# Kernel optimization log

Hardware: AMD Instinct MI355X
Metric: run time of the kernel (lower is better)

Reference implementation:

```python
import jax, jax.numpy as jnp
import numpy as np

S, B, D, V = 1024, 8, 512, 8000


def _ln(x, g, b, eps=1e-5):
    m = x.mean(-1, keepdims=True)
    v = x.var(-1, keepdims=True)
    return (x - m) / jnp.sqrt(v + eps) * g + b


def setup_inputs() -> dict:
    key = jax.random.key(0)
    ks = jax.random.split(key, 8)
    representation = jax.random.normal(ks[0], (S, B, D), jnp.float32)
    # CTC-style logits: tokens come in runs of ~4 frames so argmax has segments
    tok = jax.random.randint(ks[1], (S // 4, B), 0, V)
    tok = jnp.repeat(tok, 4, axis=0)  # [S,B]
    logit = jax.random.normal(ks[2], (S, B, V), jnp.float32) + 6.0 * jax.nn.one_hot(tok, V, dtype=jnp.float32)
    padding = jnp.zeros((B, S), bool)  # all frames valid
    # linear_adapter: Linear(D,2D) -> ReLU -> Linear(2D,D) -> LayerNorm
    w1 = jax.random.normal(ks[3], (2 * D, D), jnp.float32) * (D ** -0.5)
    b1 = jnp.zeros((2 * D,), jnp.float32)
    w2 = jax.random.normal(ks[4], (D, 2 * D), jnp.float32) * ((2 * D) ** -0.5)
    b2 = jnp.zeros((D,), jnp.float32)
    ln1_g = jnp.ones((D,), jnp.float32)
    ln1_b = jnp.zeros((D,), jnp.float32)
    # embed_adapter weight [dict_size, dim], init std = dim**-0.5
    emb_w = jax.random.normal(ks[5], (V, D), jnp.float32) * (D ** -0.5)
    eln_g = jnp.ones((D,), jnp.float32)
    eln_b = jnp.zeros((D,), jnp.float32)
    return dict(representation=representation, logit=logit, padding=padding,
                w1=w1, b1=b1, w2=w2, b2=b2, ln1_g=ln1_g, ln1_b=ln1_b,
                emb_w=emb_w, eln_g=eln_g, eln_b=eln_b)


def reference(representation, logit, padding, w1, b1, w2, b2, ln1_g, ln1_b, emb_w, eln_g, eln_b):
    # distribution = softmax(logit / T), T = 1.0
    dist = jax.nn.softmax(logit, axis=-1)  # [S,B,V]
    # linear adapter: Linear -> ReLU -> Linear -> LN
    h = jax.nn.relu(jnp.einsum('sbd,ed->sbe', representation, w1) + b1)
    linear_out = _ln(jnp.einsum('sbe,de->sbd', h, w2) + b2, ln1_g, ln1_b)
    # context adapter: dist @ embed_adapter.weight, then embed LN
    soft_out = _ln(jnp.einsum('sbv,vd->sbd', dist, emb_w), eln_g, eln_b)
    out = linear_out + soft_out  # league
    # --- CTC 'avg' compress (shrink), vectorized; output padded to S frames ---
    pred = jnp.argmax(dist, axis=-1).T  # [B,S]
    valid = ~padding  # [B,S]
    prev = jnp.concatenate([jnp.full((pred.shape[0], 1), -1, pred.dtype), pred[:, :-1]], axis=1)
    change = (pred != prev) & valid  # segment starts
    seg = jnp.cumsum(change, axis=1) - 1  # segment id per frame
    seg = jnp.where(valid, seg, S)  # invalid frames -> out-of-range id
    # weights_matrix[b, t, s] = 1/len(segment s) if frame t in segment s
    onehot = (seg[:, :, None] == jnp.arange(S)[None, None, :]).astype(out.dtype)  # [B,S,S]
    counts = onehot.sum(1)  # [B,S] frames per segment
    w = onehot * jnp.where(counts > 0, 1.0 / counts, 0.0)[:, None, :]
    # representation.permute(1,2,0).bmm(weights).permute(2,0,1)
    compressed = jnp.einsum('sbd,bst->tbd', out, w)  # [S_new(padded to S), B, D]
    new_lengths = change.sum(1)
    new_padding = jnp.arange(S)[None, :] >= new_lengths[:, None]
    return compressed, new_padding
```

## Files before the change

kernel.cpp:

```cpp
#include <hip/hip_runtime.h>
#include <hip/hip_bf16.h>

typedef __attribute__((ext_vector_type(8))) __bf16 bf16x8;
typedef __attribute__((ext_vector_type(4))) __bf16 bf16x4;
typedef __attribute__((ext_vector_type(4))) float  f32x4;

#define AS1 __attribute__((address_space(1)))
#define AS3 __attribute__((address_space(3)))

__global__ __launch_bounds__(256) void k_prep(const float* __restrict__ rep,
                                              const float* __restrict__ w1,
                                              const float* __restrict__ w2,
                                              const float* __restrict__ emb,
                                              __bf16* __restrict__ Xb,
                                              __bf16* __restrict__ w1b,
                                              __bf16* __restrict__ w2b,
                                              __bf16* __restrict__ embP) {
  int bid = blockIdx.x;
  if (bid < 5120) {
    const float* in; __bf16* out; int i;
    if (bid < 4096)      { in = rep; out = Xb;  i = bid * 256 + threadIdx.x; }
    else if (bid < 4608) { in = w1;  out = w1b; i = (bid - 4096) * 256 + threadIdx.x; }
    else                 { in = w2;  out = w2b; i = (bid - 4608) * 256 + threadIdx.x; }
    float4 f = reinterpret_cast<const float4*>(in)[i];
    bf16x4 o = { (__bf16)f.x, (__bf16)f.y, (__bf16)f.z, (__bf16)f.w };
    reinterpret_cast<bf16x4*>(out)[i] = o;
  } else {
    int idx = (bid - 5120) * 256 + threadIdx.x;
    int L = idx & 63;
    int gt = idx >> 6;
    int T = gt % 250, g = gt / 250;
    int kb = T * 32 + (L >> 4) * 8;
    int d  = g * 16 + (L & 15);
    float v[8];
#pragma unroll
    for (int j = 0; j < 8; ++j) v[j] = emb[(size_t)(kb + j) * 512 + d];
    bf16x8 o = {(__bf16)v[0], (__bf16)v[1], (__bf16)v[2], (__bf16)v[3],
                (__bf16)v[4], (__bf16)v[5], (__bf16)v[6], (__bf16)v[7]};
    *(bf16x8*)(embP + (size_t)idx * 8) = o;
  }
}

__global__ __launch_bounds__(512, 4) void k_fused(const float* __restrict__ logit,
                                                  const __bf16* __restrict__ embP,
                                                  __bf16* __restrict__ sofp,
                                                  float* __restrict__ rowsum,
                                                  float* __restrict__ amaxv,
                                                  int* __restrict__ amaxi) {
  __shared__ __align__(16) __bf16 lA[2][64 * 32];
  const int klen = 2016;
  int bid = blockIdx.x;
  int xcd = bid & 7;
  int chunk = xcd >> 1;
  int mb = ((bid >> 3) << 1) | (xcd & 1);
  int k0 = chunk * klen;
  int kn = min(klen, 8000 - k0);
  int nt = kn >> 5;
  int T0 = chunk * 63;
  int tid = threadIdx.x, lane = tid & 63, wid = tid >> 6;
  int ar = tid >> 3, ac = tid & 7;
  const float* lrow = logit + (size_t)(mb * 64 + ar) * 8000 + k0 + ac * 4;
  int awoff = ar * 64 + ((((ac >> 1) ^ ((ar >> 1) & 3)) << 4)) + (ac & 1) * 8;
  f32x4 acc[4][4] = {};
  float sumacc = 0.f, mv = -1e30f; int mi = 0;

  auto exppack = [&](float4 lg, int tt) -> bf16x4 {
    float e[4];
#pragma unroll
    for (int c = 0; c < 4; ++c) {
      float x = (&lg.x)[c];
      if (x > mv) { mv = x; mi = k0 + tt * 32 + ac * 4 + c; }
      e[c] = __expf(x);
      sumacc += e[c];
    }
    return bf16x4{ (__bf16)e[0], (__bf16)e[1], (__bf16)e[2], (__bf16)e[3] };
  };
  bf16x8 bcur[4];
  auto loadB = [&](int TT) {
#pragma unroll
    for (int n = 0; n < 4; ++n)
      bcur[n] = *(const bf16x8*)(embP + ((size_t)((wid * 4 + n) * 250 + TT)) * 512 + lane * 8);
  };

  float4 rb_ = *(const float4*)(lrow);
  float4 rb  = *(const float4*)(lrow + 32);
  loadB(T0);
  bf16x4 e0 = exppack(rb_, 0);
  *(bf16x4*)((char*)(&lA[0][0]) + awoff) = e0;

  int cur = 0;
  for (int t = 0; t < nt; ++t) {
    bool hn = (t + 1 < nt), h2 = (t + 2 < nt);
    float4 rc = rb;
    if (h2) rc = *(const float4*)(lrow + (size_t)(t + 2) * 32);
    asm volatile("s_waitcnt lgkmcnt(0)" ::: "memory");
    __builtin_amdgcn_s_barrier();
    if (hn) {
      bf16x4 e4 = exppack(rb, t + 1);
      *(bf16x4*)((char*)(&lA[cur ^ 1][0]) + awoff) = e4;
    }
    bf16x8 af[4];
#pragma unroll
    for (int m = 0; m < 4; ++m) {
      int r = m * 16 + (lane & 15);
      int s = (lane >> 4) ^ ((r >> 1) & 3);
      af[m] = *(const bf16x8*)((const char*)lA[cur] + r * 64 + s * 16);
    }
    __builtin_amdgcn_s_setprio(1);
#pragma unroll
    for (int m = 0; m < 4; ++m)
#pragma unroll
      for (int n = 0; n < 4; ++n)
        acc[m][n] = __builtin_amdgcn_mfma_f32_16x16x32_bf16(af[m], bcur[n], acc[m][n], 0, 0, 0);
    __builtin_amdgcn_s_setprio(0);
    if (hn) loadB(T0 + t + 1);
    rb = rc;
    cur ^= 1;
  }
#pragma unroll
  for (int o = 1; o <= 4; o <<= 1) {
    sumacc += __shfl_xor(sumacc, o);
    float ov = __shfl_xor(mv, o); int oi = __shfl_xor(mi, o);
    if (ov > mv || (ov == mv && oi < mi)) { mv = ov; mi = oi; }
  }
  int grow = mb * 64 + ar;
  if (ac == 0) {
    rowsum[chunk * 8192 + grow] = sumacc;
    amaxv[chunk * 8192 + grow]  = mv;
    amaxi[chunk * 8192 + grow]  = mi;
  }
  __bf16* Cb = sofp + (size_t)chunk * 8192 * 512;
  int row0 = mb * 64 + ((lane >> 4) << 2);
  int col0 = wid * 64 + (lane & 15);
#pragma unroll
  for (int n = 0; n < 4; ++n) {
    int col = col0 + n * 16;
#pragma unroll
    for (int m = 0; m < 4; ++m)
#pragma unroll
      for (int j = 0; j < 4; ++j)
        Cb[(size_t)(row0 + m * 16 + j) * 512 + col] = (__bf16)acc[m][n][j];
  }
}

template<int EPI>
__global__ __launch_bounds__(256) void k_gemm_bt(const __bf16* __restrict__ A,
                                                 const __bf16* __restrict__ B,
                                                 __bf16* __restrict__ Cb,
                                                 const float* __restrict__ bias,
                                                 int K, int N, int klen, long long ostride) {
  __shared__ __align__(16) __bf16 lA[2][128 * 64];
  __shared__ __align__(16) __bf16 lB[2][128 * 64];
  int tid = threadIdx.x, lane = tid & 63, wid = tid >> 6;
  int wr = wid >> 1, wc = wid & 1;
  int k0 = blockIdx.z * klen;
  int kn = min(klen, K - k0);
  int nt = kn >> 6;
  const __bf16* Ab = A + (size_t)blockIdx.x * 128 * K + k0;
  const __bf16* Bb = B + (size_t)blockIdx.y * 128 * K + k0;
  int sr = tid >> 3, ss = tid & 7;
  f32x4 acc[4][4] = {};

  auto stage = [&](int buf, int kt) {
#pragma unroll
    for (int i = 0; i < 4; ++i) {
      int r = i * 32 + sr;
      int col = kt + ((ss ^ (r & 7)) << 3);
      __builtin_amdgcn_global_load_lds((const AS1 void*)(Ab + (size_t)r * K + col),
                                       (AS3 void*)(&lA[buf][i * 2048 + tid * 8]), 16, 0, 0);
      __builtin_amdgcn_global_load_lds((const AS1 void*)(Bb + (size_t)r * K + col),
                                       (AS3 void*)(&lB[buf][i * 2048 + tid * 8]), 16, 0, 0);
    }
  };

  stage(0, 0);
  __syncthreads();
  int cur = 0;
  for (int t = 0; t < nt; ++t) {
    if (t + 1 < nt) stage(cur ^ 1, (t + 1) << 6);
#pragma unroll
    for (int kk = 0; kk < 2; ++kk) {
      bf16x8 af[4], bv[4];
#pragma unroll
      for (int m = 0; m < 4; ++m) {
        int r = wr * 64 + m * 16 + (lane & 15);
        int slot = ((kk << 2) + (lane >> 4)) ^ (r & 7);
        af[m] = *(const bf16x8*)((const char*)lA[cur] + r * 128 + slot * 16);
      }
#pragma unroll
      for (int n = 0; n < 4; ++n) {
        int r = wc * 64 + n * 16 + (lane & 15);
        int slot = ((kk << 2) + (lane >> 4)) ^ (r & 7);
        bv[n] = *(const bf16x8*)((const char*)lB[cur] + r * 128 + slot * 16);
      }
#pragma unroll
      for (int m = 0; m < 4; ++m)
#pragma unroll
        for (int n = 0; n < 4; ++n)
          acc[m][n] = __builtin_amdgcn_mfma_f32_16x16x32_bf16(af[m], bv[n], acc[m][n], 0, 0, 0);
    }
    __syncthreads();
    cur ^= 1;
  }
  if (EPI == 0) Cb += (size_t)blockIdx.z * (size_t)ostride;
  int row0 = blockIdx.x * 128 + wr * 64 + ((lane >> 4) << 2);
  int col0 = blockIdx.y * 128 + wc * 64 + (lane & 15);
#pragma unroll
  for (int n = 0; n < 4; ++n) {
    int col = col0 + n * 16;
    float bvv = (EPI == 1) ? bias[col] : 0.f;
#pragma unroll
    for (int m = 0; m < 4; ++m) {
#pragma unroll
      for (int j = 0; j < 4; ++j) {
        int row = row0 + m * 16 + j;
        float val = acc[m][n][j] + bvv;
        if (EPI == 1) val = fmaxf(val, 0.f);
        Cb[(size_t)row * N + col] = (__bf16)val;
      }
    }
  }
}

__global__ __launch_bounds__(256) void k_scan(const float* __restrict__ amaxv,
                                              const int* __restrict__ amaxi,
                                              int* __restrict__ seg_start,
                                              int* __restrict__ seg_cnt,
                                              int* __restrict__ new_len,
                                              float* __restrict__ out_pad) {
  __shared__ int lp[8192];
  __shared__ int len_s[8];
  int tid = threadIdx.x;
  for (int i = tid; i < 8192; i += 256) {
    float bv = amaxv[i]; int bi = amaxi[i];
#pragma unroll
    for (int c = 1; c < 4; ++c) {
      float v = amaxv[c * 8192 + i]; int ix = amaxi[c * 8192 + i];
      if (v > bv || (v == bv && ix < bi)) { bv = v; bi = ix; }
    }
    lp[(i & 7) * 1024 + (i >> 3)] = bi;
  }
  __syncthreads();
  if (tid < 8) {
    int b = tid, prev = -1, seg = -1, start = 0;
    const int* row = lp + b * 1024;
    for (int s = 0; s < 1024; ++s) {
      int p = row[s];
      if (p != prev) {
        if (seg >= 0) seg_cnt[b * 1024 + seg] = s - start;
        ++seg; seg_start[b * 1024 + seg] = s; start = s; prev = p;
      }
    }
    seg_cnt[b * 1024 + seg] = 1024 - start;
    len_s[b] = seg + 1;
    new_len[b] = seg + 1;
  }
  __syncthreads();
  for (int i = tid; i < 8192; i += 256) {
    int b = i >> 10, s = i & 1023;
    out_pad[b * 1024 + s] = (s >= len_s[b]) ? 1.f : 0.f;
  }
}

__global__ __launch_bounds__(256) void k_compress(const __bf16* __restrict__ lin,
                                                  const __bf16* __restrict__ sof,
                                                  const float* __restrict__ rowsum,
                                                  const float* __restrict__ bias2,
                                                  const float* __restrict__ g1, const float* __restrict__ b1,
                                                  const float* __restrict__ g2, const float* __restrict__ b2,
                                                  const int* __restrict__ seg_start,
                                                  const int* __restrict__ seg_cnt,
                                                  const int* __restrict__ new_len,
                                                  float* __restrict__ comp) {
  const long long P = (long long)8192 * 512;
  int wid = threadIdx.x >> 6, lane = threadIdx.x & 63;
  int t = blockIdx.x * 4 + wid, b = blockIdx.y;
  float* dst = comp + ((size_t)(t * 8 + b)) * 512 + lane * 8;
  int len = new_len[b];
  if (t >= len) {
    f32x4 z = {0.f, 0.f, 0.f, 0.f};
    *(f32x4*)dst = z; *(f32x4*)(dst + 4) = z;
    return;
  }
  int s0i = seg_start[b * 1024 + t], cnt = seg_cnt[b * 1024 + t];
  int d8 = lane * 8;
  float gg1[8], bbv1[8], gg2[8], bbv2[8], bb2v[8];
#pragma unroll
  for (int k = 0; k < 8; ++k) {
    gg1[k] = g1[d8 + k]; bbv1[k] = b1[d8 + k];
    gg2[k] = g2[d8 + k]; bbv2[k] = b2[d8 + k];
    bb2v[k] = bias2[d8 + k];
  }
  f32x4 a0 = {0.f, 0.f, 0.f, 0.f}, a1 = {0.f, 0.f, 0.f, 0.f};
  for (int s = s0i; s < s0i + cnt; ++s) {
    int row = s * 8 + b;
    size_t base = (size_t)row * 512 + d8;
    float invd = 1.f / (rowsum[row] + rowsum[8192 + row] + rowsum[16384 + row] + rowsum[24576 + row]);
    bf16x8 l0 = *(const bf16x8*)(lin + base);
    bf16x8 l1 = *(const bf16x8*)(lin + P + base);
    bf16x8 t0 = *(const bf16x8*)(sof + base);
    bf16x8 t1 = *(const bf16x8*)(sof + P + base);
    bf16x8 t2 = *(const bf16x8*)(sof + 2 * P + base);
    bf16x8 t3 = *(const bf16x8*)(sof + 3 * P + base);
    float x[8], y[8];
#pragma unroll
    for (int k = 0; k < 8; ++k) {
      x[k] = (float)l0[k] + (float)l1[k] + bb2v[k];
      y[k] = ((float)t0[k] + (float)t1[k] + (float)t2[k] + (float)t3[k]) * invd;
    }
    float sx = 0, qx = 0, sy = 0, qy = 0;
#pragma unroll
    for (int k = 0; k < 8; ++k) { sx += x[k]; qx += x[k] * x[k]; sy += y[k]; qy += y[k] * y[k]; }
#pragma unroll
    for (int o = 32; o; o >>= 1) {
      sx += __shfl_xor(sx, o); qx += __shfl_xor(qx, o);
      sy += __shfl_xor(sy, o); qy += __shfl_xor(qy, o);
    }
    const float invD = 1.f / 512.f;
    float mx = sx * invD, vx = qx * invD - mx * mx;
    float my = sy * invD, vy = qy * invD - my * my;
    float rx = rsqrtf(vx + 1e-5f), ry = rsqrtf(vy + 1e-5f);
#pragma unroll
    for (int k = 0; k < 8; ++k) {
      float o8 = (x[k] - mx) * rx * gg1[k] + bbv1[k] + (y[k] - my) * ry * gg2[k] + bbv2[k];
      if (k < 4) a0[k] += o8; else a1[k - 4] += o8;
    }
  }
  float inv = 1.f / (float)cnt;
  a0 *= inv; a1 *= inv;
  *(f32x4*)dst = a0; *(f32x4*)(dst + 4) = a1;
}

extern "C" void kernel_launch(void* const* d_in, const int* in_sizes, int n_in,
                              void* d_out, int out_size, void* d_ws, size_t ws_size,
                              hipStream_t stream) {
  const float* rep   = (const float*)d_in[0];
  const float* logit = (const float*)d_in[1];
  const float* w1    = (const float*)d_in[3];
  const float* b1    = (const float*)d_in[4];
  const float* w2    = (const float*)d_in[5];
  const float* b2    = (const float*)d_in[6];
  const float* g1    = (const float*)d_in[7];
  const float* bb1   = (const float*)d_in[8];
  const float* emb   = (const float*)d_in[9];
  const float* g2    = (const float*)d_in[10];
  const float* bb2   = (const float*)d_in[11];
  float* out = (float*)d_out;
  (void)in_sizes; (void)n_in; (void)out_size; (void)ws_size;

  char* ws = (char*)d_ws;
  size_t off = 0;
  auto alloc = [&](size_t bytes) -> void* {
    void* p = ws + off; off += (bytes + 255) & ~(size_t)255; return p;
  };
  const long long P = (long long)8192 * 512;
  __bf16* Xb    = (__bf16*)alloc((size_t)P * 2);
  __bf16* w1b   = (__bf16*)alloc((size_t)1024 * 512 * 2);
  __bf16* w2b   = (__bf16*)alloc((size_t)512 * 1024 * 2);
  __bf16* embP  = (__bf16*)alloc((size_t)512 * 8000 * 2);
  __bf16* Hb    = (__bf16*)alloc((size_t)8192 * 1024 * 2);
  __bf16* linp  = (__bf16*)alloc((size_t)P * 2 * 2);
  __bf16* sofp  = (__bf16*)alloc((size_t)P * 2 * 4);
  float*  rowsm = (float*)alloc((size_t)4 * 8192 * 4);
  float*  amv   = (float*)alloc((size_t)4 * 8192 * 4);
  int*    ami   = (int*)alloc((size_t)4 * 8192 * 4);
  int*    segs  = (int*)alloc((size_t)8192 * 4);
  int*    segc  = (int*)alloc((size_t)8192 * 4);
  int*    nlen  = (int*)alloc(64);

  k_prep<<<7120, 256, 0, stream>>>(rep, w1, w2, emb, Xb, w1b, w2b, embP);
  k_fused<<<512, 512, 0, stream>>>(logit, embP, sofp, rowsm, amv, ami);
  k_gemm_bt<1><<<dim3(64, 8, 1), 256, 0, stream>>>(Xb, w1b, Hb, b1, 512, 1024, 512, 0);
  k_gemm_bt<0><<<dim3(64, 4, 2), 256, 0, stream>>>(Hb, w2b, linp, nullptr, 1024, 512, 512, P);
  k_scan<<<1, 256, 0, stream>>>(amv, ami, segs, segc, nlen, out + (size_t)8192 * 512);
  k_compress<<<dim3(256, 8), 256, 0, stream>>>(linp, sofp, rowsm, b2, g1, bb1, g2, bb2,
                                               segs, segc, nlen, out);
}
```

Before: 281.7 us.

## Horizontally fuse softmax-embed GEMM with GEMM1, and GEMM2 with segment scan

Merges the independent kernels into shared launches. The fused softmax/embedding GEMM and the first adapter GEMM become one kernel, with blocks alternating between the two roles. The second GEMM and the argmax segment scan become another kernel, where block 0 runs the scan. This cuts launch count and per-kernel tail gaps, and lets compute-bound GEMM work overlap with the bandwidth-bound logit stream. In exchange every block of the first kernel now reserves 64KB of LDS, even the softmax path that needed only 8KB. That may reduce resident blocks per CU for the dominant logit-streaming work. GEMM1 is also retiled for 512 threads.

Measured after the change: 326.4 us. 1.16x slower.

```diff
diff --git a/kernel.cpp b/kernel.cpp
--- a/kernel.cpp
+++ b/kernel.cpp
@@ -41,224 +41,299 @@
   }
 }
 
-__global__ __launch_bounds__(512, 4) void k_fused(const float* __restrict__ logit,
-                                                  const __bf16* __restrict__ embP,
-                                                  __bf16* __restrict__ sofp,
-                                                  float* __restrict__ rowsum,
-                                                  float* __restrict__ amaxv,
-                                                  int* __restrict__ amaxi) {
-  __shared__ __align__(16) __bf16 lA[2][64 * 32];
-  const int klen = 2016;
+__global__ __launch_bounds__(512, 4) void k_fgA(const float* __restrict__ logit,
+                                                const __bf16* __restrict__ embP,
+                                                __bf16* __restrict__ sofp,
+                                                float* __restrict__ rowsum,
+                                                float* __restrict__ amaxv,
+                                                int* __restrict__ amaxi,
+                                                const __bf16* __restrict__ Xb,
+                                                const __bf16* __restrict__ w1b,
+                                                __bf16* __restrict__ Hb,
+                                                const float* __restrict__ b1) {
+  __shared__ __align__(16) __bf16 smem[4][128 * 64];
   int bid = blockIdx.x;
-  int xcd = bid & 7;
-  int chunk = xcd >> 1;
-  int mb = ((bid >> 3) << 1) | (xcd & 1);
-  int k0 = chunk * klen;
-  int kn = min(klen, 8000 - k0);
-  int nt = kn >> 5;
-  int T0 = chunk * 63;
   int tid = threadIdx.x, lane = tid & 63, wid = tid >> 6;
-  int ar = tid >> 3, ac = tid & 7;
-  const float* lrow = logit + (size_t)(mb * 64 + ar) * 8000 + k0 + ac * 4;
-  int awoff = ar * 64 + ((((ac >> 1) ^ ((ar >> 1) & 3)) << 4)) + (ac & 1) * 8;
-  f32x4 acc[4][4] = {};
-  float sumacc = 0.f, mv = -1e30f; int mi = 0;
-
-  auto exppack = [&](float4 lg, int tt) -> bf16x4 {
-    float e[4];
-#pragma unroll
-    for (int c = 0; c < 4; ++c) {
-      float x = (&lg.x)[c];
-      if (x > mv) { mv = x; mi = k0 + tt * 32 + ac * 4 + c; }
-      e[c] = __expf(x);
-      sumacc += e[c];
-    }
-    return bf16x4{ (__bf16)e[0], (__bf16)e[1], (__bf16)e[2], (__bf16)e[3] };
-  };
-  bf16x8 bcur[4];
-  auto loadB = [&](int TT) {
-#pragma unroll
-    for (int n = 0; n < 4; ++n)
-      bcur[n] = *(const bf16x8*)(embP + ((size_t)((wid * 4 + n) * 250 + TT)) * 512 + lane * 8);
-  };
-
-  float4 rb_ = *(const float4*)(lrow);
-  float4 rb  = *(const float4*)(lrow + 32);
-  loadB(T0);
-  bf16x4 e0 = exppack(rb_, 0);
-  *(bf16x4*)((char*)(&lA[0][0]) + awoff) = e0;
-
-  int cur = 0;
-  for (int t = 0; t < nt; ++t) {
-    bool hn = (t + 1 < nt), h2 = (t + 2 < nt);
-    float4 rc = rb;
-    if (h2) rc = *(const float4*)(lrow + (size_t)(t + 2) * 32);
-    asm volatile("s_waitcnt lgkmcnt(0)" ::: "memory");
-    __builtin_amdgcn_s_barrier();
-    if (hn) {
-      bf16x4 e4 = exppack(rb, t + 1);
-      *(bf16x4*)((char*)(&lA[cur ^ 1][0]) + awoff) = e4;
-    }
-    bf16x8 af[4];
-#pragma unroll
-    for (int m = 0; m < 4; ++m) {
-      int r = m * 16 + (lane & 15);
-      int s = (lane >> 4) ^ ((r >> 1) & 3);
-      af[m] = *(const bf16x8*)((const char*)lA[cur] + r * 64 + s * 16);
-    }
-    __builtin_amdgcn_s_setprio(1);
-#pragma unroll
-    for (int m = 0; m < 4; ++m)
+  int grp = bid >> 3;
+  int sub = ((grp >> 1) << 3) | (bid & 7);
+
+  if ((grp & 1) == 0) {
+    char* lAb = (char*)&smem[0][0];
+    const int klen = 2016;
+    int xcd = sub & 7;
+    int chunk = xcd >> 1;
+    int mb = ((sub >> 3) << 1) | (xcd & 1);
+    int k0 = chunk * klen;
+    int kn = min(klen, 8000 - k0);
+    int nt = kn >> 5;
+    int T0 = chunk * 63;
+    int ar = tid >> 3, ac = tid & 7;
+    const float* lrow = logit + (size_t)(mb * 64 + ar) * 8000 + k0 + ac * 4;
+    int awoff = ar * 64 + ((((ac >> 1) ^ ((ar >> 1) & 3)) << 4)) + (ac & 1) * 8;
+    f32x4 acc[4][4] = {};
+    float sumacc = 0.f, mv = -1e30f; int mi = 0;
+
+    auto exppack = [&](float4 lg, int tt) -> bf16x4 {
+      float e[4];
+#pragma unroll
+      for (int c = 0; c < 4; ++c) {
+        float x = (&lg.x)[c];
+        if (x > mv) { mv = x; mi = k0 + tt * 32 + ac * 4 + c; }
+        e[c] = __expf(x);
+        sumacc += e[c];
+      }
+      return bf16x4{ (__bf16)e[0], (__bf16)e[1], (__bf16)e[2], (__bf16)e[3] };
+    };
+    bf16x8 bcur[4];
+    auto loadB = [&](int TT) {
 #pragma unroll
       for (int n = 0; n < 4; ++n)
-        acc[m][n] = __builtin_amdgcn_mfma_f32_16x16x32_bf16(af[m], bcur[n], acc[m][n], 0, 0, 0);
-    __builtin_amdgcn_s_setprio(0);
-    if (hn) loadB(T0 + t + 1);
-    rb = rc;
-    cur ^= 1;
-  }
-#pragma unroll
-  for (int o = 1; o <= 4; o <<= 1) {
-    sumacc += __shfl_xor(sumacc, o);
-    float ov = __shfl_xor(mv, o); int oi = __shfl_xor(mi, o);
-    if (ov > mv || (ov == mv && oi < mi)) { mv = ov; mi = oi; }
-  }
-  int grow = mb * 64 + ar;
-  if (ac == 0) {
-    rowsum[chunk * 8192 + grow] = sumacc;
-    amaxv[chunk * 8192 + grow]  = mv;
-    amaxi[chunk * 8192 + grow]  = mi;
-  }
-  __bf16* Cb = sofp + (size_t)chunk * 8192 * 512;
-  int row0 = mb * 64 + ((lane >> 4) << 2);
-  int col0 = wid * 64 + (lane & 15);
-#pragma unroll
-  for (int n = 0; n < 4; ++n) {
-    int col = col0 + n * 16;
-#pragma unroll
-    for (int m = 0; m < 4; ++m)
-#pragma unroll
-      for (int j = 0; j < 4; ++j)
-        Cb[(size_t)(row0 + m * 16 + j) * 512 + col] = (__bf16)acc[m][n][j];
+        bcur[n] = *(const bf16x8*)(embP + ((size_t)((wid * 4 + n) * 250 + TT)) * 512 + lane * 8);
+    };
+
+    float4 rb_ = *(const float4*)(lrow);
+    float4 rb  = *(const float4*)(lrow + 32);
+    loadB(T0);
+    bf16x4 e0 = exppack(rb_, 0);
+    *(bf16x4*)(lAb + awoff) = e0;
+
+    int cur = 0;
+    for (int t = 0; t < nt; ++t) {
+      bool hn = (t + 1 < nt), h2 = (t + 2 < nt);
+      float4 rc = rb;
+      if (h2) rc = *(const float4*)(lrow + (size_t)(t + 2) * 32);
+      asm volatile("s_waitcnt lgkmcnt(0)" ::: "memory");
+      __builtin_amdgcn_s_barrier();
+      if (hn) {
+        bf16x4 e4 = exppack(rb, t + 1);
+        *(bf16x4*)(lAb + (cur ^ 1) * 4096 + awoff) = e4;
+      }
+      bf16x8 af[4];
+#pragma unroll
+      for (int m = 0; m < 4; ++m) {
+        int r = m * 16 + (lane & 15);
+        int s = (lane >> 4) ^ ((r >> 1) & 3);
+        af[m] = *(const bf16x8*)(lAb + cur * 4096 + r * 64 + s * 16);
+      }
+      __builtin_amdgcn_s_setprio(1);
+#pragma unroll
+      for (int m = 0; m < 4; ++m)
+#pragma unroll
+        for (int n = 0; n < 4; ++n)
+          acc[m][n] = __builtin_amdgcn_mfma_f32_16x16x32_bf16(af[m], bcur[n], acc[m][n], 0, 0, 0);
+      __builtin_amdgcn_s_setprio(0);
+      if (hn) loadB(T0 + t + 1);
+      rb = rc;
+      cur ^= 1;
+    }
+#pragma unroll
+    for (int o = 1; o <= 4; o <<= 1) {
+      sumacc += __shfl_xor(sumacc, o);
+      float ov = __shfl_xor(mv, o); int oi = __shfl_xor(mi, o);
+      if (ov > mv || (ov == mv && oi < mi)) { mv = ov; mi = oi; }
+    }
+    int grow = mb * 64 + ar;
+    if (ac == 0) {
+      rowsum[chunk * 8192 + grow] = sumacc;
+      amaxv[chunk * 8192 + grow]  = mv;
+      amaxi[chunk * 8192 + grow]  = mi;
+    }
+    __bf16* Cb = sofp + (size_t)chunk * 8192 * 512;
+    int row0 = mb * 64 + ((lane >> 4) << 2);
+    int col0 = wid * 64 + (lane & 15);
+#pragma unroll
+    for (int n = 0; n < 4; ++n) {
+      int col = col0 + n * 16;
+#pragma unroll
+      for (int m = 0; m < 4; ++m)
+#pragma unroll
+        for (int j = 0; j < 4; ++j)
+          Cb[(size_t)(row0 + m * 16 + j) * 512 + col] = (__bf16)acc[m][n][j];
+    }
+  } else {
+    __bf16* sA0 = &smem[0][0]; __bf16* sA1 = &smem[1][0];
+    __bf16* sB0 = &smem[2][0]; __bf16* sB1 = &smem[3][0];
+    int bx = sub >> 3, by = sub & 7;
+    int wr = wid >> 2, wc = wid & 3;
+    const __bf16* Ab = Xb  + (size_t)bx * 128 * 512;
+    const __bf16* Bb = w1b + (size_t)by * 128 * 512;
+    int sr = tid >> 3, ss = tid & 7;
+    f32x4 acc[4][2] = {};
+
+    auto stage = [&](__bf16* dA, __bf16* dB, int kt) {
+#pragma unroll
+      for (int i = 0; i < 2; ++i) {
+        int r = i * 64 + sr;
+        int col = kt + ((ss ^ (r & 7)) << 3);
+        __builtin_amdgcn_global_load_lds((const AS1 void*)(Ab + (size_t)r * 512 + col),
+                                         (AS3 void*)(dA + i * 4096 + tid * 8), 16, 0, 0);
+        __builtin_amdgcn_global_load_lds((const AS1 void*)(Bb + (size_t)r * 512 + col),
+                                         (AS3 void*)(dB + i * 4096 + tid * 8), 16, 0, 0);
+      }
+    };
+
+    stage(sA0, sB0, 0);
+    __syncthreads();
+    int cur = 0;
+    for (int t = 0; t < 8; ++t) {
+      if (t + 1 < 8) stage(cur ? sA0 : sA1, cur ? sB0 : sB1, (t + 1) << 6);
+      __bf16* cA = cur ? sA1 : sA0;
+      __bf16* cB = cur ? sB1 : sB0;
+#pragma unroll
+      for (int kk = 0; kk < 2; ++kk) {
+        bf16x8 af[4], bv[2];
+#pragma unroll
+        for (int m = 0; m < 4; ++m) {
+          int r = wr * 64 + m * 16 + (lane & 15);
+          int slot = ((kk << 2) + (lane >> 4)) ^ (r & 7);
+          af[m] = *(const bf16x8*)((const char*)cA + r * 128 + slot * 16);
+        }
+#pragma unroll
+        for (int n = 0; n < 2; ++n) {
+          int r = wc * 32 + n * 16 + (lane & 15);
+          int slot = ((kk << 2) + (lane >> 4)) ^ (r & 7);
+          bv[n] = *(const bf16x8*)((const char*)cB + r * 128 + slot * 16);
+        }
+#pragma unroll
+        for (int m = 0; m < 4; ++m)
+#pragma unroll
+          for (int n = 0; n < 2; ++n)
+            acc[m][n] = __builtin_amdgcn_mfma_f32_16x16x32_bf16(af[m], bv[n], acc[m][n], 0, 0, 0);
+      }
+      __syncthreads();
+      cur ^= 1;
+    }
+    int row0 = bx * 128 + wr * 64 + ((lane >> 4) << 2);
+    int col0 = by * 128 + wc * 32 + (lane & 15);
+#pragma unroll
+    for (int n = 0; n < 2; ++n) {
+      int col = col0 + n * 16;
+      float bvv = b1[col];
+#pragma unroll
+      for (int m = 0; m < 4; ++m) {
+#pragma unroll
+        for (int j = 0; j < 4; ++j) {
+          int row = row0 + m * 16 + j;
+          float val = fmaxf(acc[m][n][j] + bvv, 0.f);
+          Hb[(size_t)row * 1024 + col] = (__bf16)val;
+        }
+      }
+    }
   }
 }
 
-template<int EPI>
-__global__ __launch_bounds__(256) void k_gemm_bt(const __bf16* __restrict__ A,
-                                                 const __bf16* __restrict__ B,
-                                                 __bf16* __restrict__ Cb,
-                                                 const float* __restrict__ bias,
-                                                 int K, int N, int klen, long long ostride) {
-  __shared__ __align__(16) __bf16 lA[2][128 * 64];
-  __shared__ __align__(16) __bf16 lB[2][128 * 64];
+__global__ __launch_bounds__(256) void k_gsB(const __bf16* __restrict__ Hb,
+                                             const __bf16* __restrict__ w2b,
+                                             __bf16* __restrict__ linp,
+                                             const float* __restrict__ amaxv,
+                                             const int* __restrict__ amaxi,
+                                             int* __restrict__ seg_start,
+                                             int* __restrict__ seg_cnt,
+                                             int* __restrict__ new_len,
+                                             float* __restrict__ out_pad) {
+  __shared__ __align__(16) __bf16 smem[4][128 * 64];
+  const long long P = (long long)8192 * 512;
+  int bid = blockIdx.x;
   int tid = threadIdx.x, lane = tid & 63, wid = tid >> 6;
-  int wr = wid >> 1, wc = wid & 1;
-  int k0 = blockIdx.z * klen;
-  int kn = min(klen, K - k0);
-  int nt = kn >> 6;
-  const __bf16* Ab = A + (size_t)blockIdx.x * 128 * K + k0;
-  const __bf16* Bb = B + (size_t)blockIdx.y * 128 * K + k0;
-  int sr = tid >> 3, ss = tid & 7;
-  f32x4 acc[4][4] = {};
-
-  auto stage = [&](int buf, int kt) {
-#pragma unroll
-    for (int i = 0; i < 4; ++i) {
-      int r = i * 32 + sr;
-      int col = kt + ((ss ^ (r & 7)) << 3);
-      __builtin_amdgcn_global_load_lds((const AS1 void*)(Ab + (size_t)r * K + col),
-                                       (AS3 void*)(&lA[buf][i * 2048 + tid * 8]), 16, 0, 0);
-      __builtin_amdgcn_global_load_lds((const AS1 void*)(Bb + (size_t)r * K + col),
-                                       (AS3 void*)(&lB[buf][i * 2048 + tid * 8]), 16, 0, 0);
-    }
-  };
-
-  stage(0, 0);
-  __syncthreads();
-  int cur = 0;
-  for (int t = 0; t < nt; ++t) {
-    if (t + 1 < nt) stage(cur ^ 1, (t + 1) << 6);
-#pragma unroll
-    for (int kk = 0; kk < 2; ++kk) {
-      bf16x8 af[4], bv[4];
-#pragma unroll
-      for (int m = 0; m < 4; ++m) {
-        int r = wr * 64 + m * 16 + (lane & 15);
-        int slot = ((kk << 2) + (lane >> 4)) ^ (r & 7);
-        af[m] = *(const bf16x8*)((const char*)lA[cur] + r * 128 + slot * 16);
-      }
-#pragma unroll
-      for (int n = 0; n < 4; ++n) {
-        int r = wc * 64 + n * 16 + (lane & 15);
-        int slot = ((kk << 2) + (lane >> 4)) ^ (r & 7);
-        bv[n] = *(const bf16x8*)((const char*)lB[cur] + r * 128 + slot * 16);
-      }
+  if (bid == 0) {
+    int* lp = (int*)&smem[0][0];
+    int* len_s = lp + 8192;
+    for (int i = tid; i < 8192; i += 256) {
+      float bv = amaxv[i]; int bi = amaxi[i];
+#pragma unroll
+      for (int c = 1; c < 4; ++c) {
+        float v = amaxv[c * 8192 + i]; int ix = amaxi[c * 8192 + i];
+        if (v > bv || (v == bv && ix < bi)) { bv = v; bi = ix; }
+      }
+      lp[(i & 7) * 1024 + (i >> 3)] = bi;
+    }
+    __syncthreads();
+    if (tid < 8) {
+      int b = tid, prev = -1, seg = -1, start = 0;
+      const int* row = lp + b * 1024;
+      for (int s = 0; s < 1024; ++s) {
+        int p = row[s];
+        if (p != prev) {
+          if (seg >= 0) seg_cnt[b * 1024 + seg] = s - start;
+          ++seg; seg_start[b * 1024 + seg] = s; start = s; prev = p;
+        }
+      }
+      seg_cnt[b * 1024 + seg] = 1024 - start;
+      len_s[b] = seg + 1;
+      new_len[b] = seg + 1;
+    }
+    __syncthreads();
+    for (int i = tid; i < 8192; i += 256) {
+      int b = i >> 10, s = i & 1023;
+      out_pad[b * 1024 + s] = (s >= len_s[b]) ? 1.f : 0.f;
+    }
+  } else {
+    int gbid = bid - 1;
+    int z = gbid >> 8, y = (gbid >> 6) & 3, x = gbid & 63;
+    __bf16* sA0 = &smem[0][0]; __bf16* sA1 = &smem[1][0];
+    __bf16* sB0 = &smem[2][0]; __bf16* sB1 = &smem[3][0];
+    int wr = wid >> 1, wc = wid & 1;
+    int k0 = z * 512;
+    const __bf16* Ab = Hb  + (size_t)x * 128 * 1024 + k0;
+    const __bf16* Bb = w2b + (size_t)y * 128 * 1024 + k0;
+    int sr = tid >> 3, ss = tid & 7;
+    f32x4 acc[4][4] = {};
+
+    auto stage = [&](__bf16* dA, __bf16* dB, int kt) {
+#pragma unroll
+      for (int i = 0; i < 4; ++i) {
+        int r = i * 32 + sr;
+        int col = kt + ((ss ^ (r & 7)) << 3);
+        __builtin_amdgcn_global_load_lds((const AS1 void*)(Ab + (size_t)r * 1024 + col),
+                                         (AS3 void*)(dA + i * 2048 + tid * 8), 16, 0, 0);
+        __builtin_amdgcn_global_load_lds((const AS1 void*)(Bb + (size_t)r * 1024 + col),
+                                         (AS3 void*)(dB + i * 2048 + tid * 8), 16, 0, 0);
+      }
+    };
+
+    stage(sA0, sB0, 0);
+    __syncthreads();
+    int cur = 0;
+    for (int t = 0; t < 8; ++t) {
+      if (t + 1 < 8) stage(cur ? sA0 : sA1, cur ? sB0 : sB1, (t + 1) << 6);
+      __bf16* cA = cur ? sA1 : sA0;
+      __bf16* cB = cur ? sB1 : sB0;
+#pragma unroll
+      for (int kk = 0; kk < 2; ++kk) {
+        bf16x8 af[4], bv[4];
+#pragma unroll
+        for (int m = 0; m < 4; ++m) {
+          int r = wr * 64 + m * 16 + (lane & 15);
+          int slot = ((kk << 2) + (lane >> 4)) ^ (r & 7);
+          af[m] = *(const bf16x8*)((const char*)cA + r * 128 + slot * 16);
+        }
+#pragma unroll
+        for (int n = 0; n < 4; ++n) {
+          int r = wc * 64 + n * 16 + (lane & 15);
+          int slot = ((kk << 2) + (lane >> 4)) ^ (r & 7);
+          bv[n] = *(const bf16x8*)((const char*)cB + r * 128 + slot * 16);
+        }
+#pragma unroll
+        for (int m = 0; m < 4; ++m)
+#pragma unroll
+          for (int n = 0; n < 4; ++n)
+            acc[m][n] = __builtin_amdgcn_mfma_f32_16x16x32_bf16(af[m], bv[n], acc[m][n], 0, 0, 0);
+      }
+      __syncthreads();
+      cur ^= 1;
+    }
+    __bf16* Cb = linp + (size_t)z * (size_t)P;
+    int row0 = x * 128 + wr * 64 + ((lane >> 4) << 2);
+    int col0 = y * 128 + wc * 64 + (lane & 15);
+#pragma unroll
+    for (int n = 0; n < 4; ++n) {
+      int col = col0 + n * 16;
 #pragma unroll
       for (int m = 0; m < 4; ++m)
 #pragma unroll
-        for (int n = 0; n < 4; ++n)
-          acc[m][n] = __builtin_amdgcn_mfma_f32_16x16x32_bf16(af[m], bv[n], acc[m][n], 0, 0, 0);
-    }
-    __syncthreads();
-    cur ^= 1;
-  }
-  if (EPI == 0) Cb += (size_t)blockIdx.z * (size_t)ostride;
-  int row0 = blockIdx.x * 128 + wr * 64 + ((lane >> 4) << 2);
-  int col0 = blockIdx.y * 128 + wc * 64 + (lane & 15);
-#pragma unroll
-  for (int n = 0; n < 4; ++n) {
-    int col = col0 + n * 16;
-    float bvv = (EPI == 1) ? bias[col] : 0.f;
-#pragma unroll
-    for (int m = 0; m < 4; ++m) {
-#pragma unroll
-      for (int j = 0; j < 4; ++j) {
-        int row = row0 + m * 16 + j;
-        float val = acc[m][n][j] + bvv;
-        if (EPI == 1) val = fmaxf(val, 0.f);
-        Cb[(size_t)row * N + col] = (__bf16)val;
-      }
-    }
-  }
-}
-
-__global__ __launch_bounds__(256) void k_scan(const float* __restrict__ amaxv,
-                                              const int* __restrict__ amaxi,
-                                              int* __restrict__ seg_start,
-                                              int* __restrict__ seg_cnt,
-                                              int* __restrict__ new_len,
-                                              float* __restrict__ out_pad) {
-  __shared__ int lp[8192];
-  __shared__ int len_s[8];
-  int tid = threadIdx.x;
-  for (int i = tid; i < 8192; i += 256) {
-    float bv = amaxv[i]; int bi = amaxi[i];
-#pragma unroll
-    for (int c = 1; c < 4; ++c) {
-      float v = amaxv[c * 8192 + i]; int ix = amaxi[c * 8192 + i];
-      if (v > bv || (v == bv && ix < bi)) { bv = v; bi = ix; }
-    }
-    lp[(i & 7) * 1024 + (i >> 3)] = bi;
-  }
-  __syncthreads();
-  if (tid < 8) {
-    int b = tid, prev = -1, seg = -1, start = 0;
-    const int* row = lp + b * 1024;
-    for (int s = 0; s < 1024; ++s) {
-      int p = row[s];
-      if (p != prev) {
-        if (seg >= 0) seg_cnt[b * 1024 + seg] = s - start;
-        ++seg; seg_start[b * 1024 + seg] = s; start = s; prev = p;
-      }
-    }
-    seg_cnt[b * 1024 + seg] = 1024 - start;
-    len_s[b] = seg + 1;
-    new_len[b] = seg + 1;
-  }
-  __syncthreads();
-  for (int i = tid; i < 8192; i += 256) {
-    int b = i >> 10, s = i & 1023;
-    out_pad[b * 1024 + s] = (s >= len_s[b]) ? 1.f : 0.f;
+        for (int j = 0; j < 4; ++j)
+          Cb[(size_t)(row0 + m * 16 + j) * 512 + col] = (__bf16)acc[m][n][j];
+    }
   }
 }
 
@@ -369,10 +444,9 @@
   int*    nlen  = (int*)alloc(64);
 
   k_prep<<<7120, 256, 0, stream>>>(rep, w1, w2, emb, Xb, w1b, w2b, embP);
-  k_fused<<<512, 512, 0, stream>>>(logit, embP, sofp, rowsm, amv, ami);
-  k_gemm_bt<1><<<dim3(64, 8, 1), 256, 0, stream>>>(Xb, w1b, Hb, b1, 512, 1024, 512, 0);
-  k_gemm_bt<0><<<dim3(64, 4, 2), 256, 0, stream>>>(Hb, w2b, linp, nullptr, 1024, 512, 512, P);
-  k_scan<<<1, 256, 0, stream>>>(amv, ami, segs, segc, nlen, out + (size_t)8192 * 512);
+  k_fgA<<<1024, 512, 0, stream>>>(logit, embP, sofp, rowsm, amv, ami, Xb, w1b, Hb, b1);
+  k_gsB<<<513, 256, 0, stream>>>(Hb, w2b, linp, amv, ami, segs, segc, nlen,
+                                 out + (size_t)8192 * 512);
   k_compress<<<dim3(256, 8), 256, 0, stream>>>(linp, sofp, rowsm, b2, g1, bb1, g2, bb2,
                                                segs, segc, nlen, out);
 }
```
